# Optimization experiments

Hardware: AMD Instinct MI355X
Metric: run time of the kernel (lower is better)

## Reference

```python
import jax, jax.numpy as jnp
import numpy as np

N = 100000
E = 1600000
IN_CH = 64
EDGE_DIM = 32
OUT_CH = 64
HEADS = 4
HEAD_CH = OUT_CH // HEADS
NEG_SLOPE = 0.2


def setup_inputs() -> dict:
    key = jax.random.key(0)
    k1, k2, k3, k4, k5 = jax.random.split(key, 5)
    x = jax.random.normal(k1, (N, IN_CH), dtype=jnp.float32)
    edge_index = jax.random.randint(k2, (2, E), 0, N, dtype=jnp.int64)
    edge_feature = jax.random.normal(k3, (E, EDGE_DIM), dtype=jnp.float32)
    # linear_msg: Linear(in_channels + edge_dim, out_channels, bias=False); torch weight is [out, in]
    W_msg = jax.random.normal(k4, (OUT_CH, IN_CH + EDGE_DIM), dtype=jnp.float32) * (1.0 / np.sqrt(IN_CH + EDGE_DIM))
    # att_msg: [1, heads, head_channels], glorot init
    att_msg = jax.random.normal(k5, (1, HEADS, HEAD_CH), dtype=jnp.float32) * np.sqrt(2.0 / (HEADS + HEAD_CH))
    return {"x": x, "edge_index": edge_index, "edge_feature": edge_feature, "W_msg": W_msg, "att_msg": att_msg}


def reference(x, edge_index, edge_feature, W_msg, att_msg):
    src = edge_index[0]  # x_j (source, gathered for messages)
    dst = edge_index[1]  # x_i / edge_index_i (softmax + aggregation groups)
    # per-edge gather + concat + linear (no bias)
    msg = jnp.concatenate([x[src], edge_feature], axis=-1) @ W_msg.T  # [E, OUT_CH]
    msg = msg.reshape(-1, HEADS, HEAD_CH)  # [E, H, Dh]
    # attention logits per head
    alpha = jnp.sum(msg * att_msg, axis=-1)  # [E, H]
    alpha = jnp.where(alpha >= 0, alpha, NEG_SLOPE * alpha)  # leaky_relu
    # segment softmax over destination nodes (PyG softmax: subtract max, / (sum + 1e-16))
    seg_max = jax.ops.segment_max(alpha, dst, num_segments=N)  # [N, H]
    alpha = jnp.exp(alpha - seg_max[dst])
    seg_sum = jax.ops.segment_sum(alpha, dst, num_segments=N)  # [N, H]
    alpha = alpha / (seg_sum[dst] + 1e-16)
    # weighted scatter-add aggregation (aggr='add', norm is None)
    out = jax.ops.segment_sum(msg * alpha[..., None], dst, num_segments=N)  # [N, H, Dh]
    return out.reshape(N, OUT_CH)
```

## Files before the change

kernel.cpp:

```cpp
#include <hip/hip_runtime.h>
#include <cstdint>
#include <cstddef>

constexpr int NN   = 100000;
constexpr int NE   = 1600000;
constexpr int CIN  = 64;
constexpr int CE   = 32;
constexpr int CCAT = 96;
constexpr int COUT = 64;
constexpr int NH   = 4;

constexpr int SCAN_B = 512;
constexpr int NBLK   = (NN + SCAN_B - 1) / SCAN_B;

constexpr int SLOTS_PER_WAVE = 64;

__global__ void k_watt(const float* __restrict__ W, const float* __restrict__ att,
                       float* __restrict__ watt) {
  int t = blockIdx.x * blockDim.x + threadIdx.x;
  if (t < NH * CCAT) {
    int h = t / CCAT, k = t - h * CCAT;
    float s = 0.f;
#pragma unroll
    for (int d = 0; d < 16; ++d)
      s += att[h * 16 + d] * W[(h * 16 + d) * CCAT + k];
    watt[t] = s;
  }
}

__global__ __launch_bounds__(256) void k_xw(const float* __restrict__ x,
                                            const float* __restrict__ W,
                                            const float* __restrict__ watt,
                                            float* __restrict__ xw,
                                            float* __restrict__ xa) {
  int n = blockIdx.x * 256 + threadIdx.x;
  if (n >= NN) return;
  float xi[CIN];
  const float4* xp = reinterpret_cast<const float4*>(x + (size_t)n * CIN);
#pragma unroll
  for (int j = 0; j < CIN / 4; ++j) {
    float4 v = xp[j];
    xi[4 * j + 0] = v.x; xi[4 * j + 1] = v.y;
    xi[4 * j + 2] = v.z; xi[4 * j + 3] = v.w;
  }
  float4* xwp = reinterpret_cast<float4*>(xw + (size_t)n * COUT);
  for (int d0 = 0; d0 < COUT; d0 += 4) {
    float a0 = 0.f, a1 = 0.f, a2 = 0.f, a3 = 0.f;
#pragma unroll
    for (int k = 0; k < CIN; ++k) {
      float xv = xi[k];
      a0 += xv * W[(d0 + 0) * CCAT + k];
      a1 += xv * W[(d0 + 1) * CCAT + k];
      a2 += xv * W[(d0 + 2) * CCAT + k];
      a3 += xv * W[(d0 + 3) * CCAT + k];
    }
    xwp[d0 >> 2] = make_float4(a0, a1, a2, a3);
  }
#pragma unroll
  for (int h = 0; h < NH; ++h) {
    float a = 0.f;
#pragma unroll
    for (int k = 0; k < CIN; ++k) a += xi[k] * watt[h * CCAT + k];
    xa[n * NH + h] = a;
  }
}

__global__ __launch_bounds__(256) void k_hist(const int* __restrict__ ei,
                                              int* __restrict__ deg) {
  int e = blockIdx.x * 256 + threadIdx.x;
  if (e < NE) atomicAdd(&deg[ei[NE + e]], 1);
}

__global__ __launch_bounds__(SCAN_B) void k_scan1(const int* __restrict__ deg,
                                                  int* __restrict__ iscan,
                                                  int* __restrict__ bsum) {
  __shared__ int lds[SCAN_B];
  int t = threadIdx.x, i = blockIdx.x * SCAN_B + t;
  int v = (i < NN) ? deg[i] : 0;
  lds[t] = v;
  __syncthreads();
  for (int off = 1; off < SCAN_B; off <<= 1) {
    int u = (t >= off) ? lds[t - off] : 0;
    __syncthreads();
    lds[t] += u;
    __syncthreads();
  }
  if (i < NN) iscan[i] = lds[t];
  if (t == SCAN_B - 1) bsum[blockIdx.x] = lds[t];
}

__global__ __launch_bounds__(256) void k_scan2(const int* __restrict__ bsum,
                                               int* __restrict__ boff) {
  __shared__ int lds[256];
  int t = threadIdx.x;
  int v = (t < NBLK) ? bsum[t] : 0;
  lds[t] = v;
  __syncthreads();
  for (int off = 1; off < 256; off <<= 1) {
    int u = (t >= off) ? lds[t - off] : 0;
    __syncthreads();
    lds[t] += u;
    __syncthreads();
  }
  if (t < NBLK) boff[t] = lds[t] - v;
}

__global__ __launch_bounds__(256) void k_scan3(const int* __restrict__ iscan,
                                               const int* __restrict__ deg,
                                               const int* __restrict__ boff,
                                               int* __restrict__ start,
                                               int* __restrict__ cursor) {
  int i = blockIdx.x * 256 + threadIdx.x;
  if (i < NN) {
    int s = iscan[i] - deg[i] + boff[i / SCAN_B];
    start[i] = s;
    cursor[i] = s;
  }
  if (i == 0) start[NN] = NE;
}

__global__ __launch_bounds__(256) void k_edge(const int* __restrict__ ei,
                                              const float* __restrict__ ef,
                                              const float* __restrict__ watt,
                                              const float* __restrict__ xa,
                                              int* __restrict__ cursor,
                                              float* __restrict__ rec) {
  int e = blockIdx.x * 256 + threadIdx.x;
  if (e >= NE) return;
  int src = ei[e];
  int dst = ei[NE + e];

  float f[CE];
  const float4* fp = reinterpret_cast<const float4*>(ef + (size_t)e * CE);
#pragma unroll
  for (int j = 0; j < CE / 4; ++j) {
    float4 v = fp[j];
    f[4 * j + 0] = v.x; f[4 * j + 1] = v.y;
    f[4 * j + 2] = v.z; f[4 * j + 3] = v.w;
  }
  float4 xav = *reinterpret_cast<const float4*>(xa + (size_t)src * NH);
  float a[NH] = {xav.x, xav.y, xav.z, xav.w};
#pragma unroll
  for (int h = 0; h < NH; ++h) {
    float acc = a[h];
#pragma unroll
    for (int k = 0; k < CE; ++k)
      acc += f[k] * watt[h * CCAT + CIN + k];
    a[h] = (acc >= 0.f) ? acc : 0.2f * acc;
  }

  int slot = atomicAdd(&cursor[dst], 1);
  float4* rp = reinterpret_cast<float4*>(rec + (size_t)slot * 8);
  float4 meta;
  meta.x = __int_as_float(e);
  meta.y = __int_as_float(src);
  meta.z = __int_as_float(dst);
  meta.w = 0.f;
  rp[0] = meta;
  rp[1] = make_float4(a[0], a[1], a[2], a[3]);
}

__global__ __launch_bounds__(256) void k_norm(const int* __restrict__ start,
                                              float* __restrict__ rec) {
  int t = blockIdx.x * 256 + threadIdx.x;
  int n = t >> 2, h = t & 3;
  if (n >= NN) return;
  int s0 = start[n], s1 = start[n + 1];
  float m = -INFINITY;
  for (int s = s0; s < s1; ++s)
    m = fmaxf(m, rec[(size_t)s * 8 + 4 + h]);
  float sum = 0.f;
  for (int s = s0; s < s1; ++s) {
    float p = __expf(rec[(size_t)s * 8 + 4 + h] - m);
    rec[(size_t)s * 8 + 4 + h] = p;
    sum += p;
  }
  float rs = 1.f / (sum + 1e-16f);
  for (int s = s0; s < s1; ++s)
    rec[(size_t)s * 8 + 4 + h] *= rs;
}

__global__ __launch_bounds__(256) void k_agg(const float* __restrict__ rec,
                                             const float* __restrict__ ef,
                                             const float* __restrict__ W,
                                             const float* __restrict__ xw,
                                             float* __restrict__ out) {
  int gw = blockIdx.x * 4 + (threadIdx.x >> 6);
  int lane = threadIdx.x & 63;
  int h = lane >> 4;

  float Wr[CE];
  const float4* wrp = reinterpret_cast<const float4*>(W + (size_t)lane * CCAT + CIN);
#pragma unroll
  for (int j = 0; j < CE / 4; ++j) {
    float4 v = wrp[j];
    Wr[4 * j + 0] = v.x; Wr[4 * j + 1] = v.y;
    Wr[4 * j + 2] = v.z; Wr[4 * j + 3] = v.w;
  }

  const float4* rp = reinterpret_cast<const float4*>(rec);
  size_t sbase = (size_t)gw * SLOTS_PER_WAVE;

  float acc = 0.f;
  int cur = -1;
#pragma unroll 4
  for (int i = 0; i < SLOTS_PER_WAVE; ++i) {
    size_t s = sbase + i;
    float4 meta = rp[2 * s];
    float4 p4   = rp[2 * s + 1];
    int e   = __builtin_amdgcn_readfirstlane(__float_as_int(meta.x));
    int src = __builtin_amdgcn_readfirstlane(__float_as_int(meta.y));
    int dst = __builtin_amdgcn_readfirstlane(__float_as_int(meta.z));

    if (dst != cur) {
      if (cur >= 0) atomicAdd(&out[(size_t)cur * COUT + lane], acc);
      acc = 0.f;
      cur = dst;
    }

    float pw = (h & 2) ? ((h & 1) ? p4.w : p4.z)
                       : ((h & 1) ? p4.y : p4.x);

    float msg = xw[(size_t)src * COUT + lane];
    const float4* efp = reinterpret_cast<const float4*>(ef + (size_t)e * CE);
#pragma unroll
    for (int j = 0; j < CE / 4; ++j) {
      float4 v = efp[j];
      msg += v.x * Wr[4 * j + 0] + v.y * Wr[4 * j + 1] +
             v.z * Wr[4 * j + 2] + v.w * Wr[4 * j + 3];
    }
    acc += pw * msg;
  }
  atomicAdd(&out[(size_t)cur * COUT + lane], acc);
}

extern "C" void kernel_launch(void* const* d_in, const int* in_sizes, int n_in,
                              void* d_out, int out_size, void* d_ws, size_t ws_size,
                              hipStream_t stream) {
  const float* x   = (const float*)d_in[0];
  const int*   ei  = (const int*)d_in[1];
  const float* ef  = (const float*)d_in[2];
  const float* W   = (const float*)d_in[3];
  const float* att = (const float*)d_in[4];
  float* out = (float*)d_out;

  char* ws = (char*)d_ws;
  float* xw     = (float*)(ws + 0);
  float* xa     = (float*)(ws + 25600000);
  float* watt   = (float*)(ws + 27200000);
  int*   start  = (int*)  (ws + 27202048);
  float* rec    = (float*)(ws + 27602176);
  int*   deg    = (int*)  (ws + 78802176);
  int*   iscan  = (int*)  (ws + 79202176);
  int*   cursor = (int*)  (ws + 79602176);
  int*   bsum   = (int*)  (ws + 80002176);
  int*   boff   = (int*)  (ws + 80003200);

  hipMemsetAsync(deg, 0, (size_t)NN * 4, stream);
  hipMemsetAsync(out, 0, (size_t)NN * COUT * 4, stream);

  k_watt<<<1, 384, 0, stream>>>(W, att, watt);
  k_xw<<<(NN + 255) / 256, 256, 0, stream>>>(x, W, watt, xw, xa);
  k_hist<<<(NE + 255) / 256, 256, 0, stream>>>(ei, deg);
  k_scan1<<<NBLK, SCAN_B, 0, stream>>>(deg, iscan, bsum);
  k_scan2<<<1, 256, 0, stream>>>(bsum, boff);
  k_scan3<<<(NN + 255) / 256, 256, 0, stream>>>(iscan, deg, boff, start, cursor);
  k_edge<<<(NE + 255) / 256, 256, 0, stream>>>(ei, ef, watt, xa, cursor, rec);
  k_norm<<<(NN * NH + 255) / 256, 256, 0, stream>>>(start, rec);
  k_agg<<<(NE / SLOTS_PER_WAVE) / 4, 256, 0, stream>>>(rec, ef, W, xw, out);
}
```

Measured before the change: 874.6 us.

## Fuse segment softmax into per-node aggregation and factor edge-feature projection

Drops the separate normalization kernel and the slot-chunked atomic aggregation. Each wave now owns one destination node: it computes the max, exponentials and sum inline, and writes output directly, so the atomics and the output memset go away. The edge-feature linear term is restructured so that the attention-weighted edge features are aggregated per head first and then projected once per node through shared memory, rather than once per edge. The cost is that work per wave now varies with node degree, each wave makes two passes over its records, and load balance across waves is worse.

```diff
diff --git a/kernel.cpp b/kernel.cpp
--- a/kernel.cpp
+++ b/kernel.cpp
@@ -12,8 +12,6 @@
 
 constexpr int SCAN_B = 512;
 constexpr int NBLK   = (NN + SCAN_B - 1) / SCAN_B;
-
-constexpr int SLOTS_PER_WAVE = 64;
 
 __global__ void k_watt(const float* __restrict__ W, const float* __restrict__ att,
                        float* __restrict__ watt) {
@@ -160,37 +158,22 @@
   rp[1] = make_float4(a[0], a[1], a[2], a[3]);
 }
 
-__global__ __launch_bounds__(256) void k_norm(const int* __restrict__ start,
-                                              float* __restrict__ rec) {
-  int t = blockIdx.x * 256 + threadIdx.x;
-  int n = t >> 2, h = t & 3;
-  if (n >= NN) return;
-  int s0 = start[n], s1 = start[n + 1];
-  float m = -INFINITY;
-  for (int s = s0; s < s1; ++s)
-    m = fmaxf(m, rec[(size_t)s * 8 + 4 + h]);
-  float sum = 0.f;
-  for (int s = s0; s < s1; ++s) {
-    float p = __expf(rec[(size_t)s * 8 + 4 + h] - m);
-    rec[(size_t)s * 8 + 4 + h] = p;
-    sum += p;
-  }
-  float rs = 1.f / (sum + 1e-16f);
-  for (int s = s0; s < s1; ++s)
-    rec[(size_t)s * 8 + 4 + h] *= rs;
-}
-
-__global__ __launch_bounds__(256) void k_agg(const float* __restrict__ rec,
+__global__ __launch_bounds__(256) void k_agg(const int* __restrict__ start,
+                                             const float* __restrict__ rec,
                                              const float* __restrict__ ef,
                                              const float* __restrict__ W,
                                              const float* __restrict__ xw,
                                              float* __restrict__ out) {
-  int gw = blockIdx.x * 4 + (threadIdx.x >> 6);
-  int lane = threadIdx.x & 63;
-  int h = lane >> 4;
+  __shared__ float efs[4 * 4 * 36];
+  int wv = threadIdx.x >> 6;
+  int l = threadIdx.x & 63;
+  float* my = efs + wv * (4 * 36);
+  int h = l >> 4;
+  int k = l & 31;
+  bool b16 = (l & 16) != 0, b32 = (l & 32) != 0;
 
   float Wr[CE];
-  const float4* wrp = reinterpret_cast<const float4*>(W + (size_t)lane * CCAT + CIN);
+  const float4* wrp = reinterpret_cast<const float4*>(W + (size_t)l * CCAT + CIN);
 #pragma unroll
   for (int j = 0; j < CE / 4; ++j) {
     float4 v = wrp[j];
@@ -198,40 +181,56 @@
     Wr[4 * j + 2] = v.z; Wr[4 * j + 3] = v.w;
   }
 
-  const float4* rp = reinterpret_cast<const float4*>(rec);
-  size_t sbase = (size_t)gw * SLOTS_PER_WAVE;
-
-  float acc = 0.f;
-  int cur = -1;
-#pragma unroll 4
-  for (int i = 0; i < SLOTS_PER_WAVE; ++i) {
-    size_t s = sbase + i;
-    float4 meta = rp[2 * s];
-    float4 p4   = rp[2 * s + 1];
-    int e   = __builtin_amdgcn_readfirstlane(__float_as_int(meta.x));
-    int src = __builtin_amdgcn_readfirstlane(__float_as_int(meta.y));
-    int dst = __builtin_amdgcn_readfirstlane(__float_as_int(meta.z));
-
-    if (dst != cur) {
-      if (cur >= 0) atomicAdd(&out[(size_t)cur * COUT + lane], acc);
-      acc = 0.f;
-      cur = dst;
-    }
-
-    float pw = (h & 2) ? ((h & 1) ? p4.w : p4.z)
-                       : ((h & 1) ? p4.y : p4.x);
-
-    float msg = xw[(size_t)src * COUT + lane];
-    const float4* efp = reinterpret_cast<const float4*>(ef + (size_t)e * CE);
+  for (int n = blockIdx.x * 4 + wv; n < NN; n += gridDim.x * 4) {
+    int s0 = start[n], s1 = start[n + 1];
+
+    float m0 = -INFINITY, m1 = -INFINITY, m2 = -INFINITY, m3 = -INFINITY;
+    for (int s = s0; s < s1; ++s) {
+      float4 lg = *reinterpret_cast<const float4*>(rec + (size_t)s * 8 + 4);
+      m0 = fmaxf(m0, lg.x); m1 = fmaxf(m1, lg.y);
+      m2 = fmaxf(m2, lg.z); m3 = fmaxf(m3, lg.w);
+    }
+    float mw  = b32 ? (b16 ? m3 : m2) : (b16 ? m1 : m0);
+    float me0 = b32 ? m2 : m0;
+    float me1 = b32 ? m3 : m1;
+
+    float acc = 0.f, ssum = 0.f, ea0 = 0.f, ea1 = 0.f;
+    for (int s = s0; s < s1; ++s) {
+      float4 mt = *reinterpret_cast<const float4*>(rec + (size_t)s * 8);
+      float4 lg = *reinterpret_cast<const float4*>(rec + (size_t)s * 8 + 4);
+      int e   = __float_as_int(mt.x);
+      int src = __float_as_int(mt.y);
+      float lw  = b32 ? (b16 ? lg.w : lg.z) : (b16 ? lg.y : lg.x);
+      float le0 = b32 ? lg.z : lg.x;
+      float le1 = b32 ? lg.w : lg.y;
+      float pw  = __expf(lw - mw);
+      float pe0 = __expf(le0 - me0);
+      float pe1 = __expf(le1 - me1);
+      float efv = ef[(size_t)e * CE + k];
+      float xv  = xw[(size_t)src * COUT + l];
+      acc  += pw * xv;
+      ssum += pw;
+      ea0  += pe0 * efv;
+      ea1  += pe1 * efv;
+    }
+
+    int hp2 = b32 ? 2 : 0;
+    my[(hp2 + 0) * 36 + k] = ea0;
+    my[(hp2 + 1) * 36 + k] = ea1;
+    asm volatile("s_waitcnt lgkmcnt(0)" ::: "memory");
+
+    float efwe = 0.f;
+    const float4* mp = reinterpret_cast<const float4*>(my + h * 36);
 #pragma unroll
     for (int j = 0; j < CE / 4; ++j) {
-      float4 v = efp[j];
-      msg += v.x * Wr[4 * j + 0] + v.y * Wr[4 * j + 1] +
-             v.z * Wr[4 * j + 2] + v.w * Wr[4 * j + 3];
-    }
-    acc += pw * msg;
-  }
-  atomicAdd(&out[(size_t)cur * COUT + lane], acc);
+      float4 v = mp[j];
+      efwe += v.x * Wr[4 * j + 0] + v.y * Wr[4 * j + 1] +
+              v.z * Wr[4 * j + 2] + v.w * Wr[4 * j + 3];
+    }
+
+    float rs = 1.f / (ssum + 1e-16f);
+    out[(size_t)n * COUT + l] = (acc + efwe) * rs;
+  }
 }
 
 extern "C" void kernel_launch(void* const* d_in, const int* in_sizes, int n_in,
@@ -257,7 +256,6 @@
   int*   boff   = (int*)  (ws + 80003200);
 
   hipMemsetAsync(deg, 0, (size_t)NN * 4, stream);
-  hipMemsetAsync(out, 0, (size_t)NN * COUT * 4, stream);
 
   k_watt<<<1, 384, 0, stream>>>(W, att, watt);
   k_xw<<<(NN + 255) / 256, 256, 0, stream>>>(x, W, watt, xw, xa);
@@ -266,6 +264,5 @@
   k_scan2<<<1, 256, 0, stream>>>(bsum, boff);
   k_scan3<<<(NN + 255) / 256, 256, 0, stream>>>(iscan, deg, boff, start, cursor);
   k_edge<<<(NE + 255) / 256, 256, 0, stream>>>(ei, ef, watt, xa, cursor, rec);
-  k_norm<<<(NN * NH + 255) / 256, 256, 0, stream>>>(start, rec);
-  k_agg<<<(NE / SLOTS_PER_WAVE) / 4, 256, 0, stream>>>(rec, ef, W, xw, out);
-}
+  k_agg<<<2048, 256, 0, stream>>>(start, rec, ef, W, xw, out);
+}
```

Measured after the change: 812.7 us. 7.1% less time.
